# Optimization experiments

Hardware: AMD Instinct MI355X
Metric: run time of the kernel (lower is better)

## Reference

```python
import jax, jax.numpy as jnp
import numpy as np

# per-position segment id for seq_len=16: slices [0:1],[1:6],[6:9],[9:10],[10:16]
SEG = np.array([0] + [1]*5 + [2]*3 + [3] + [4]*6, dtype=np.int32)
HEAD_DIM = 3
NUM_HEADS = 2


def setup_inputs() -> dict:
    key = jax.random.key(0)
    ks = jax.random.split(key, 9)
    B = 262144
    s = 1.0 / np.sqrt(6.0)  # torch Linear init scale
    return {
        "x": jax.random.normal(ks[0], (B, 16, 6), dtype=jnp.float32),
        "Wq": jax.random.uniform(ks[1], (5, 6, 6), jnp.float32, -s, s),
        "bq": jax.random.uniform(ks[2], (5, 6), jnp.float32, -s, s),
        "Wk": jax.random.uniform(ks[3], (5, 6, 6), jnp.float32, -s, s),
        "bk": jax.random.uniform(ks[4], (5, 6), jnp.float32, -s, s),
        "Wv": jax.random.uniform(ks[5], (5, 6, 6), jnp.float32, -s, s),
        "bv": jax.random.uniform(ks[6], (5, 6), jnp.float32, -s, s),
        "Wo": jax.random.uniform(ks[7], (6, 6), jnp.float32, -s, s),
        "bo": jax.random.uniform(ks[8], (6,), jnp.float32, -s, s),
    }


def reference(x, Wq, bq, Wk, bk, Wv, bv, Wo, bo):
    B, S, D = x.shape  # S=16, D=6
    seg = jnp.asarray(SEG)

    def seg_proj(W, b):
        # torch Linear: y = x @ W.T + b; gather per-position segment weights
        return jnp.einsum('bsd,sod->bso', x, W[seg]) + b[seg]

    def heads(t):
        return t.reshape(B, S, NUM_HEADS, HEAD_DIM).transpose(0, 2, 1, 3)

    Q = heads(seg_proj(Wq, bq))  # [B,H,S,hd]
    K = heads(seg_proj(Wk, bk))
    V = heads(seg_proj(Wv, bv))

    scores = jnp.einsum('bhqd,bhkd->bhqk', Q, K) / jnp.sqrt(jnp.float32(HEAD_DIM))
    attn = jax.nn.softmax(scores, axis=-1)
    ctx = jnp.einsum('bhqk,bhkd->bhqd', attn, V)
    ctx = ctx.transpose(0, 2, 1, 3).reshape(B, S, D)
    return ctx @ Wo.T + bo
```

## Files before the change

kernel.cpp:

```cpp
#include <hip/hip_runtime.h>

#define QSCALE 0.83294038f

#define GSTRIDE 196
#define WAVE_FLOATS 784
#define MAXBLOCKS 2048

__device__ __forceinline__ void proj6(const float* wp, const float* bp,
                                      float x0, float x1, float x2,
                                      float x3, float x4, float x5,
                                      float r[6])
{
    float w[36];
    const float4* p = (const float4*)wp;
    #pragma unroll
    for (int i = 0; i < 9; ++i) {
        float4 v = p[i];
        w[i*4+0] = v.x; w[i*4+1] = v.y; w[i*4+2] = v.z; w[i*4+3] = v.w;
    }
    float bb[6];
    const float2* b2 = (const float2*)bp;
    #pragma unroll
    for (int i = 0; i < 3; ++i) { float2 v = b2[i]; bb[i*2] = v.x; bb[i*2+1] = v.y; }
    #pragma unroll
    for (int j = 0; j < 6; ++j) {
        r[j] = bb[j] + x0*w[j*6+0] + x1*w[j*6+1] + x2*w[j*6+2]
                     + x3*w[j*6+3] + x4*w[j*6+4] + x5*w[j*6+5];
    }
}

__global__ __launch_bounds__(256) void attn_seg_kernel(
    const float* __restrict__ x,
    const float* __restrict__ Wq, const float* __restrict__ bq,
    const float* __restrict__ Wk, const float* __restrict__ bk,
    const float* __restrict__ Wv, const float* __restrict__ bv,
    const float* __restrict__ Wo, const float* __restrict__ bo,
    float* __restrict__ out, int total)
{
    __shared__ __align__(16) float lds[4 * WAVE_FLOATS];
    const int t   = threadIdx.x;
    const int wv_ = t >> 6;
    const int g   = (t >> 4) & 3;
    const int s   = t & 15;
    const int seg = (s == 0) ? 0 : (s < 6) ? 1 : (s < 9) ? 2 : (s == 9) ? 3 : 4;

    float* const kvg = &lds[wv_ * WAVE_FLOATS + g * GSTRIDE];
    float* const kvw = kvg + s * 12;

    const float* const wqb = Wq + seg * 36;
    const float* const wkb = Wk + seg * 36;
    const float* const wvb = Wv + seg * 36;
    const float* const bqb = bq + seg * 6;
    const float* const bkb = bk + seg * 6;
    const float* const bvb = bv + seg * 6;

    const int ntiles = (total + 255) >> 8;

    int tile = blockIdx.x;
    float x0=0.f,x1=0.f,x2=0.f,x3=0.f,x4=0.f,x5=0.f;
    {
        const int pos = (tile << 8) + t;
        if (pos < total) {
            const float* xp = x + (size_t)pos * 6;
            float2 a = *(const float2*)(xp);
            float2 b = *(const float2*)(xp + 2);
            float2 c = *(const float2*)(xp + 4);
            x0=a.x; x1=a.y; x2=b.x; x3=b.y; x4=c.x; x5=c.y;
        }
    }

    #pragma unroll 1
    for (; tile < ntiles; ) {
        const int pos   = (tile << 8) + t;
        const bool valid = pos < total;
        const int ntile = tile + gridDim.x;

        float nx0=0.f,nx1=0.f,nx2=0.f,nx3=0.f,nx4=0.f,nx5=0.f;
        if (ntile < ntiles) {
            const int npos = (ntile << 8) + t;
            if (npos < total) {
                const float* xp = x + (size_t)npos * 6;
                float2 a = *(const float2*)(xp);
                float2 b = *(const float2*)(xp + 2);
                float2 c = *(const float2*)(xp + 4);
                nx0=a.x; nx1=a.y; nx2=b.x; nx3=b.y; nx4=c.x; nx5=c.y;
            }
        }

        float kk[6], vvv[6], q[6];
        {
            const float* wp = wkb; const float* bp = bkb;
            asm volatile("" : "+v"(wp), "+v"(bp));
            proj6(wp, bp, x0,x1,x2,x3,x4,x5, kk);
        }
        {
            const float* wp = wvb; const float* bp = bvb;
            asm volatile("" : "+v"(wp), "+v"(bp));
            proj6(wp, bp, x0,x1,x2,x3,x4,x5, vvv);
        }
        {
            const float* wp = wqb; const float* bp = bqb;
            asm volatile("" : "+v"(wp), "+v"(bp));
            proj6(wp, bp, x0,x1,x2,x3,x4,x5, q);
        }
        #pragma unroll
        for (int i = 0; i < 6; ++i) q[i] *= QSCALE;

        *(float4*)(kvw)     = make_float4(kk[0], kk[1], kk[2], kk[3]);
        *(float4*)(kvw + 4) = make_float4(kk[4], kk[5], vvv[0], vvv[1]);
        *(float4*)(kvw + 8) = make_float4(vvv[2], vvv[3], vvv[4], vvv[5]);

        __builtin_amdgcn_wave_barrier();
        asm volatile("s_waitcnt lgkmcnt(0)" ::: "memory");
        __builtin_amdgcn_sched_barrier(0);

        float s0 = 0.f, s1 = 0.f;
        float c0=0.f,c1=0.f,c2=0.f,c3=0.f,c4=0.f,c5=0.f;
        #pragma unroll
        for (int k = 0; k < 16; ++k) {
            float4 a = *(const float4*)(kvg + k * 12);
            float4 b = *(const float4*)(kvg + k * 12 + 4);
            float4 c = *(const float4*)(kvg + k * 12 + 8);
            float e0 = __builtin_amdgcn_exp2f(q[0]*a.x + q[1]*a.y + q[2]*a.z);
            float e1 = __builtin_amdgcn_exp2f(q[3]*a.w + q[4]*b.x + q[5]*b.y);
            s0 += e0; s1 += e1;
            c0 += e0*b.z; c1 += e0*b.w; c2 += e0*c.x;
            c3 += e1*c.y; c4 += e1*c.z; c5 += e1*c.w;
        }
        const float i0 = __builtin_amdgcn_rcpf(s0);
        const float i1 = __builtin_amdgcn_rcpf(s1);
        c0 *= i0; c1 *= i0; c2 *= i0;
        c3 *= i1; c4 *= i1; c5 *= i1;

        float o_[6];
        #pragma unroll
        for (int i = 0; i < 6; ++i) {
            o_[i] = bo[i] + c0*Wo[i*6+0] + c1*Wo[i*6+1] + c2*Wo[i*6+2]
                          + c3*Wo[i*6+3] + c4*Wo[i*6+4] + c5*Wo[i*6+5];
        }
        if (valid) {
            float* op = out + (size_t)pos * 6;
            *(float2*)(op)     = make_float2(o_[0], o_[1]);
            *(float2*)(op + 2) = make_float2(o_[2], o_[3]);
            *(float2*)(op + 4) = make_float2(o_[4], o_[5]);
        }

        __builtin_amdgcn_wave_barrier();

        x0=nx0; x1=nx1; x2=nx2; x3=nx3; x4=nx4; x5=nx5;
        tile = ntile;
    }
}

extern "C" void kernel_launch(void* const* d_in, const int* in_sizes, int n_in,
                              void* d_out, int out_size, void* d_ws, size_t ws_size,
                              hipStream_t stream) {
    const float* x  = (const float*)d_in[0];
    const float* Wq = (const float*)d_in[1];
    const float* bq = (const float*)d_in[2];
    const float* Wk = (const float*)d_in[3];
    const float* bk = (const float*)d_in[4];
    const float* Wv = (const float*)d_in[5];
    const float* bv = (const float*)d_in[6];
    const float* Wo = (const float*)d_in[7];
    const float* bo = (const float*)d_in[8];
    float* out = (float*)d_out;

    const int total  = in_sizes[0] / 6;
    const int ntiles = (total + 255) / 256;
    const int grid   = ntiles < MAXBLOCKS ? ntiles : MAXBLOCKS;
    attn_seg_kernel<<<grid, 256, 0, stream>>>(x, Wq, bq, Wk, bk, Wv, bv, Wo, bo, out, total);
}
```

Measured before the change: 260.7 us.

## Hoist per-segment QKV weights into registers and size grid by occupancy

Loads each thread's segment Q/K/V weights and biases into registers once before the persistent loop, folding the softmax scale into the Q weights, so they are no longer reloaded from memory every tile. Sets launch bounds to 256 threads with a minimum of 2 blocks per CU, and sizes the persistent grid from the occupancy query and CU count instead of a fixed cap of 2048. About 130 extra registers per thread may lower occupancy or cause spills, and a smaller grid means fewer waves to hide memory latency.

```diff
diff --git a/kernel.cpp b/kernel.cpp
--- a/kernel.cpp
+++ b/kernel.cpp
@@ -4,32 +4,8 @@
 
 #define GSTRIDE 196
 #define WAVE_FLOATS 784
-#define MAXBLOCKS 2048
 
-__device__ __forceinline__ void proj6(const float* wp, const float* bp,
-                                      float x0, float x1, float x2,
-                                      float x3, float x4, float x5,
-                                      float r[6])
-{
-    float w[36];
-    const float4* p = (const float4*)wp;
-    #pragma unroll
-    for (int i = 0; i < 9; ++i) {
-        float4 v = p[i];
-        w[i*4+0] = v.x; w[i*4+1] = v.y; w[i*4+2] = v.z; w[i*4+3] = v.w;
-    }
-    float bb[6];
-    const float2* b2 = (const float2*)bp;
-    #pragma unroll
-    for (int i = 0; i < 3; ++i) { float2 v = b2[i]; bb[i*2] = v.x; bb[i*2+1] = v.y; }
-    #pragma unroll
-    for (int j = 0; j < 6; ++j) {
-        r[j] = bb[j] + x0*w[j*6+0] + x1*w[j*6+1] + x2*w[j*6+2]
-                     + x3*w[j*6+3] + x4*w[j*6+4] + x5*w[j*6+5];
-    }
-}
-
-__global__ __launch_bounds__(256) void attn_seg_kernel(
+__global__ __launch_bounds__(256, 2) void attn_seg_kernel(
     const float* __restrict__ x,
     const float* __restrict__ Wq, const float* __restrict__ bq,
     const float* __restrict__ Wk, const float* __restrict__ bk,
@@ -47,37 +23,52 @@
     float* const kvg = &lds[wv_ * WAVE_FLOATS + g * GSTRIDE];
     float* const kvw = kvg + s * 12;
 
-    const float* const wqb = Wq + seg * 36;
-    const float* const wkb = Wk + seg * 36;
-    const float* const wvb = Wv + seg * 36;
-    const float* const bqb = bq + seg * 6;
-    const float* const bkb = bk + seg * 6;
-    const float* const bvb = bv + seg * 6;
-
-    const int ntiles = (total + 255) >> 8;
-
-    int tile = blockIdx.x;
-    float x0=0.f,x1=0.f,x2=0.f,x3=0.f,x4=0.f,x5=0.f;
+    float wqr[36], wkr[36], wvr[36], bqr[6], bkr[6], bvr[6];
     {
-        const int pos = (tile << 8) + t;
-        if (pos < total) {
-            const float* xp = x + (size_t)pos * 6;
-            float2 a = *(const float2*)(xp);
-            float2 b = *(const float2*)(xp + 2);
-            float2 c = *(const float2*)(xp + 4);
-            x0=a.x; x1=a.y; x2=b.x; x3=b.y; x4=c.x; x5=c.y;
+        const float4* pq = (const float4*)(Wq + seg * 36);
+        const float4* pk = (const float4*)(Wk + seg * 36);
+        const float4* pv = (const float4*)(Wv + seg * 36);
+        #pragma unroll
+        for (int i = 0; i < 9; ++i) {
+            float4 a = pq[i];
+            wqr[i*4+0] = a.x * QSCALE; wqr[i*4+1] = a.y * QSCALE;
+            wqr[i*4+2] = a.z * QSCALE; wqr[i*4+3] = a.w * QSCALE;
+            float4 b = pk[i];
+            wkr[i*4+0] = b.x; wkr[i*4+1] = b.y; wkr[i*4+2] = b.z; wkr[i*4+3] = b.w;
+            float4 c = pv[i];
+            wvr[i*4+0] = c.x; wvr[i*4+1] = c.y; wvr[i*4+2] = c.z; wvr[i*4+3] = c.w;
+        }
+        const float2* q2 = (const float2*)(bq + seg * 6);
+        const float2* k2 = (const float2*)(bk + seg * 6);
+        const float2* v2 = (const float2*)(bv + seg * 6);
+        #pragma unroll
+        for (int i = 0; i < 3; ++i) {
+            float2 a = q2[i]; bqr[i*2] = a.x * QSCALE; bqr[i*2+1] = a.y * QSCALE;
+            float2 b = k2[i]; bkr[i*2] = b.x; bkr[i*2+1] = b.y;
+            float2 c = v2[i]; bvr[i*2] = c.x; bvr[i*2+1] = c.y;
         }
     }
 
+    const int step = (int)gridDim.x << 8;
+    int base = (int)blockIdx.x << 8;
+
+    float x0=0.f,x1=0.f,x2=0.f,x3=0.f,x4=0.f,x5=0.f;
+    if (base + t < total) {
+        const float* xp = x + (size_t)(base + t) * 6;
+        float2 a = *(const float2*)(xp);
+        float2 b = *(const float2*)(xp + 2);
+        float2 c = *(const float2*)(xp + 4);
+        x0=a.x; x1=a.y; x2=b.x; x3=b.y; x4=c.x; x5=c.y;
+    }
+
     #pragma unroll 1
-    for (; tile < ntiles; ) {
-        const int pos   = (tile << 8) + t;
+    for (; base < total; base += step) {
+        const int pos = base + t;
         const bool valid = pos < total;
-        const int ntile = tile + gridDim.x;
 
         float nx0=0.f,nx1=0.f,nx2=0.f,nx3=0.f,nx4=0.f,nx5=0.f;
-        if (ntile < ntiles) {
-            const int npos = (ntile << 8) + t;
+        {
+            const int npos = base + step + t;
             if (npos < total) {
                 const float* xp = x + (size_t)npos * 6;
                 float2 a = *(const float2*)(xp);
@@ -87,28 +78,25 @@
             }
         }
 
-        float kk[6], vvv[6], q[6];
-        {
-            const float* wp = wkb; const float* bp = bkb;
-            asm volatile("" : "+v"(wp), "+v"(bp));
-            proj6(wp, bp, x0,x1,x2,x3,x4,x5, kk);
+        float kk[6], vvv[6];
+        #pragma unroll
+        for (int j = 0; j < 6; ++j) {
+            kk[j] = bkr[j] + x0*wkr[j*6+0] + x1*wkr[j*6+1] + x2*wkr[j*6+2]
+                           + x3*wkr[j*6+3] + x4*wkr[j*6+4] + x5*wkr[j*6+5];
+            vvv[j] = bvr[j] + x0*wvr[j*6+0] + x1*wvr[j*6+1] + x2*wvr[j*6+2]
+                            + x3*wvr[j*6+3] + x4*wvr[j*6+4] + x5*wvr[j*6+5];
         }
-        {
-            const float* wp = wvb; const float* bp = bvb;
-            asm volatile("" : "+v"(wp), "+v"(bp));
-            proj6(wp, bp, x0,x1,x2,x3,x4,x5, vvv);
-        }
-        {
-            const float* wp = wqb; const float* bp = bqb;
-            asm volatile("" : "+v"(wp), "+v"(bp));
-            proj6(wp, bp, x0,x1,x2,x3,x4,x5, q);
-        }
-        #pragma unroll
-        for (int i = 0; i < 6; ++i) q[i] *= QSCALE;
 
         *(float4*)(kvw)     = make_float4(kk[0], kk[1], kk[2], kk[3]);
         *(float4*)(kvw + 4) = make_float4(kk[4], kk[5], vvv[0], vvv[1]);
         *(float4*)(kvw + 8) = make_float4(vvv[2], vvv[3], vvv[4], vvv[5]);
+
+        float q[6];
+        #pragma unroll
+        for (int j = 0; j < 6; ++j) {
+            q[j] = bqr[j] + x0*wqr[j*6+0] + x1*wqr[j*6+1] + x2*wqr[j*6+2]
+                          + x3*wqr[j*6+3] + x4*wqr[j*6+4] + x5*wqr[j*6+5];
+        }
 
         __builtin_amdgcn_wave_barrier();
         asm volatile("s_waitcnt lgkmcnt(0)" ::: "memory");
@@ -148,7 +136,6 @@
         __builtin_amdgcn_wave_barrier();
 
         x0=nx0; x1=nx1; x2=nx2; x3=nx3; x4=nx4; x5=nx5;
-        tile = ntile;
     }
 }
 
@@ -168,6 +155,18 @@
 
     const int total  = in_sizes[0] / 6;
     const int ntiles = (total + 255) / 256;
-    const int grid   = ntiles < MAXBLOCKS ? ntiles : MAXBLOCKS;
+
+    static int grid_cap = 0;
+    if (grid_cap == 0) {
+        int bpc = 0;
+        if (hipOccupancyMaxActiveBlocksPerMultiprocessor(&bpc, attn_seg_kernel, 256, 0)
+                != hipSuccess || bpc <= 0) bpc = 2;
+        hipDeviceProp_t prop;
+        int ncu = 256;
+        if (hipGetDeviceProperties(&prop, 0) == hipSuccess && prop.multiProcessorCount > 0)
+            ncu = prop.multiProcessorCount;
+        grid_cap = bpc * ncu;
+    }
+    const int grid = ntiles < grid_cap ? ntiles : grid_cap;
     attn_seg_kernel<<<grid, 256, 0, stream>>>(x, Wq, bq, Wk, bk, Wv, bv, Wo, bo, out, total);
 }
```

After: 338.6 us. 1.3x slower.
